# Optimization experiments

Hardware: AMD Instinct MI355X
Metric: run time of the kernel (lower is better)

## Reference

```python
import jax, jax.numpy as jnp
import numpy as np

BN_EPS = 1e-5


def _conv1x1(x, w, b):
    # x: (B,C,H,W), w: (O,C) -> (B,O,H,W)
    return jnp.einsum('bchw,oc->bohw', x, w) + b[None, :, None, None]


def _maxpool2x2(x):
    b, c, h, w = x.shape
    return x.reshape(b, c, h // 2, 2, w // 2, 2).max(axis=(3, 5))


def _minmax(a, axis):
    mn = a.min(axis=axis, keepdims=True)
    mx = a.max(axis=axis, keepdims=True)
    return (a - mn) / (mx - mn)


def _gaussian_bias(row, dh, dw):
    # Vectorized version of the original per-row numpy double loop.
    sigma = max(1, int(min(dh, dw) / 10))
    j = jnp.arange(row)
    cx = ((j // 4) // dw).astype(jnp.float32)   # floor(j/4/down_col)
    cy = ((j // 4) % dw).astype(jnp.float32)    # floor(j/4) % down_col
    mx = jnp.arange(dh, dtype=jnp.float32)[None, :, None]
    my = jnp.arange(dw, dtype=jnp.float32)[None, None, :]
    d2 = (mx - cx[:, None, None]) ** 2 + (my - cy[:, None, None]) ** 2
    return (-d2 / (2.0 * sigma * sigma)).reshape(row, dh * dw)  # (row, col)


def reference(x, g_w, g_b, theta_w, theta_b, phi_w, phi_b, w_w, w_b,
              bn_gamma, bn_beta, bn_mean, bn_var):
    b, c, H, W = x.shape
    ic = g_w.shape[0]
    dh, dw = H // 2, W // 2
    row, col = H * W, dh * dw

    g_x = _maxpool2x2(_conv1x1(x, g_w, g_b)).reshape(b, ic, col).transpose(0, 2, 1)  # (b,col,ic)
    theta = _conv1x1(x, theta_w, theta_b).reshape(b, ic, row).transpose(0, 2, 1)     # (b,row,ic)
    phi = _maxpool2x2(_conv1x1(x, phi_w, phi_b)).reshape(b, ic, col)                 # (b,ic,col)

    f = jnp.einsum('bri,bic->brc', theta, phi)  # (b,row,col)
    temp = _gaussian_bias(row, dh, dw)[None]    # (1,row,col), same for all batch

    f = (_minmax(f, -1) - 1.0) + (_minmax(temp, -1) - 1.0)
    f_div_C = jax.nn.softmax(f, axis=-1)

    g_x = _minmax(g_x, 1)  # min/max over positions
    y = jnp.einsum('brc,bci->bri', f_div_C, g_x)        # (b,row,ic)
    y = y.transpose(0, 2, 1).reshape(b, ic, H, W)

    W_y = _conv1x1(y, w_w, w_b)
    W_y = bn_gamma[None, :, None, None] * (W_y - bn_mean[None, :, None, None]) \
        * jax.lax.rsqrt(bn_var + BN_EPS)[None, :, None, None] + bn_beta[None, :, None, None]
    return W_y + x


def setup_inputs() -> dict:
    key = jax.random.key(0)
    ks = jax.random.split(key, 13)
    B, C, IC, H, W = 8, 64, 32, 64, 64
    s = 0.1
    return {
        'x': jax.random.normal(ks[0], (B, C, H, W), jnp.float32),
        'g_w': jax.random.normal(ks[1], (IC, C), jnp.float32) * s,
        'g_b': jax.random.normal(ks[2], (IC,), jnp.float32) * s,
        'theta_w': jax.random.normal(ks[3], (IC, C), jnp.float32) * s,
        'theta_b': jax.random.normal(ks[4], (IC,), jnp.float32) * s,
        'phi_w': jax.random.normal(ks[5], (IC, C), jnp.float32) * s,
        'phi_b': jax.random.normal(ks[6], (IC,), jnp.float32) * s,
        'w_w': jax.random.normal(ks[7], (C, IC), jnp.float32) * s,
        'w_b': jax.random.normal(ks[8], (C,), jnp.float32) * s,
        'bn_gamma': jax.random.uniform(ks[9], (C,), jnp.float32, 0.5, 1.5),
        'bn_beta': jax.random.normal(ks[10], (C,), jnp.float32) * s,
        'bn_mean': jax.random.normal(ks[11], (C,), jnp.float32) * s,
        'bn_var': jax.random.uniform(ks[12], (C,), jnp.float32, 0.5, 1.5),
    }
```

## Files before the change

kernel.cpp:

```cpp
#include <hip/hip_runtime.h>
#include <math.h>

#define RFL(x) __builtin_amdgcn_readfirstlane(x)

static constexpr int Bn = 8, Cn = 64, ICn = 32, Hn = 64, Wn = 64;
static constexpr int ROW = Hn * Wn;
static constexpr int COLn = 1024;

static constexpr size_t OFF_THETA = 0;
static constexpr size_t OFF_PHI   = (size_t)Bn * ROW * ICn;
static constexpr size_t OFF_G     = OFF_PHI + (size_t)Bn * ICn * COLn;
static constexpr size_t OFF_Y     = OFF_G + (size_t)Bn * COLn * ICn;
static constexpr size_t OFF_GMN   = OFF_Y + (size_t)Bn * ROW * ICn;
static constexpr size_t OFF_GINV  = OFF_GMN + (size_t)Bn * ICn;

__device__ __forceinline__ void gload_lds16(const float* src, float* ldsbase) {
    __builtin_amdgcn_global_load_lds(
        (const __attribute__((address_space(1))) unsigned int*)(const void*)src,
        (__attribute__((address_space(3))) unsigned int*)(void*)ldsbase, 16, 0, 0);
}

__global__ __launch_bounds__(256) void k_conv3(
    const float* __restrict__ x,
    const float* __restrict__ wth, const float* __restrict__ bth,
    const float* __restrict__ wph, const float* __restrict__ bph,
    const float* __restrict__ wg,  const float* __restrict__ bg,
    float* __restrict__ theta, float* __restrict__ phi, float* __restrict__ g)
{
    const int tid  = threadIdx.x;
    const int lane = tid & 63;
    const int ty   = RFL(tid >> 6);
    const int b    = blockIdx.z;
    const int pc   = blockIdx.x * 64 + lane;
    const int phh  = pc >> 5, pww = pc & 31;
    const int o0   = (blockIdx.y * 4 + ty) * 4;

    const float* xb = x + (size_t)b * Cn * ROW;
    const int pos0 = (2 * phh) * Wn + 2 * pww;

    float accT[4][4], accP[4][4], accG[4][4];
    #pragma unroll
    for (int j = 0; j < 4; ++j)
        #pragma unroll
        for (int q = 0; q < 4; ++q) { accT[j][q] = 0.f; accP[j][q] = 0.f; accG[j][q] = 0.f; }

    float2 pf0[8], pf1[8];
    #pragma unroll
    for (int i = 0; i < 8; ++i) {
        const float* xc = xb + (size_t)i * ROW + pos0;
        pf0[i] = *(const float2*)xc;
        pf1[i] = *(const float2*)(xc + Wn);
    }
    #pragma unroll 1
    for (int cb = 0; cb < Cn; cb += 8) {
        float2 c0[8], c1[8];
        #pragma unroll
        for (int i = 0; i < 8; ++i) { c0[i] = pf0[i]; c1[i] = pf1[i]; }
        if (cb + 8 < Cn) {
            #pragma unroll
            for (int i = 0; i < 8; ++i) {
                const float* xc = xb + (size_t)(cb + 8 + i) * ROW + pos0;
                pf0[i] = *(const float2*)xc;
                pf1[i] = *(const float2*)(xc + Wn);
            }
        }
        #pragma unroll
        for (int i = 0; i < 8; ++i) {
            const int c = cb + i;
            const float xv0 = c0[i].x, xv1 = c0[i].y, xv2 = c1[i].x, xv3 = c1[i].y;
            #pragma unroll
            for (int j = 0; j < 4; ++j) {
                const int o = o0 + j;
                const float wt  = wth[o * Cn + c];
                const float wp  = wph[o * Cn + c];
                const float wgv = wg [o * Cn + c];
                accT[j][0] = fmaf(wt, xv0, accT[j][0]); accT[j][1] = fmaf(wt, xv1, accT[j][1]);
                accT[j][2] = fmaf(wt, xv2, accT[j][2]); accT[j][3] = fmaf(wt, xv3, accT[j][3]);
                accP[j][0] = fmaf(wp, xv0, accP[j][0]); accP[j][1] = fmaf(wp, xv1, accP[j][1]);
                accP[j][2] = fmaf(wp, xv2, accP[j][2]); accP[j][3] = fmaf(wp, xv3, accP[j][3]);
                accG[j][0] = fmaf(wgv, xv0, accG[j][0]); accG[j][1] = fmaf(wgv, xv1, accG[j][1]);
                accG[j][2] = fmaf(wgv, xv2, accG[j][2]); accG[j][3] = fmaf(wgv, xv3, accG[j][3]);
            }
        }
    }

    const int prow[4] = {pos0, pos0 + 1, pos0 + Wn, pos0 + Wn + 1};
    const float4 bt4 = *(const float4*)(bth + o0);
    #pragma unroll
    for (int q = 0; q < 4; ++q) {
        float4 tv;
        tv.x = accT[0][q] + bt4.x; tv.y = accT[1][q] + bt4.y;
        tv.z = accT[2][q] + bt4.z; tv.w = accT[3][q] + bt4.w;
        *(float4*)&theta[((size_t)b * ROW + prow[q]) * ICn + o0] = tv;
    }
    float4 gv;
    #pragma unroll
    for (int j = 0; j < 4; ++j) {
        const int o = o0 + j;
        float mp = fmaxf(fmaxf(accP[j][0], accP[j][1]), fmaxf(accP[j][2], accP[j][3]));
        phi[((size_t)b * ICn + o) * COLn + pc] = mp + bph[o];
        float mg = fmaxf(fmaxf(accG[j][0], accG[j][1]), fmaxf(accG[j][2], accG[j][3]));
        (&gv.x)[j] = mg + bg[o];
    }
    *(float4*)&g[((size_t)b * COLn + pc) * ICn + o0] = gv;
}

__global__ __launch_bounds__(64) void k_gminmax(
    const float* __restrict__ g, float* __restrict__ gmn, float* __restrict__ ginv)
{
    const int ic = blockIdx.x, b = blockIdx.y, lane = threadIdx.x;
    float mn = 3.4e38f, mx = -3.4e38f;
    for (int i = 0; i < COLn; i += 64) {
        float v = g[((size_t)b * COLn + i + lane) * ICn + ic];
        mn = fminf(mn, v); mx = fmaxf(mx, v);
    }
    #pragma unroll
    for (int m = 1; m < 64; m <<= 1) {
        mn = fminf(mn, __shfl_xor(mn, m));
        mx = fmaxf(mx, __shfl_xor(mx, m));
    }
    if (lane == 0) {
        gmn[b * ICn + ic] = mn;
        ginv[b * ICn + ic] = 1.0f / (mx - mn);
    }
}

#define RPW 4
#define CCH 256
#define PCOL(c) ((c) ^ ((((c) >> 5) & 7) << 2))

__global__ __launch_bounds__(256, 5) void k_attn(
    const float* __restrict__ theta, const float* __restrict__ phi,
    const float* __restrict__ g, const float* __restrict__ gmn,
    const float* __restrict__ ginv, float* __restrict__ y)
{
    __shared__ float smem[32 * CCH];

    const int tid  = threadIdx.x;
    const int lane = tid & 63;
    const int wid  = RFL(tid >> 6);
    const int b    = blockIdx.y;
    const int icq  = lane & 7;
    const int csplit = lane >> 3;
    const int colbase = lane * 4;

    const float* phiB = phi + (size_t)b * ICn * COLn;
    const float* gB   = g + (size_t)b * COLn * ICn;
    const float4 gmn4 = *(const float4*)(gmn + b * ICn + icq * 4);
    const float4 giv4 = *(const float4*)(ginv + b * ICn + icq * 4);

    const int row0 = blockIdx.x * 16 + wid * RPW;
    const float* thB = theta + ((size_t)b * ROW + row0) * ICn;
    float* const pSw = smem + wid * (RPW * CCH);

    float4 f4[RPW][4];
    #pragma unroll
    for (int r = 0; r < RPW; ++r) {
        f4[r][0] = make_float4(0.f, 0.f, 0.f, 0.f);
        f4[r][1] = make_float4(0.f, 0.f, 0.f, 0.f);
        f4[r][2] = make_float4(0.f, 0.f, 0.f, 0.f);
        f4[r][3] = make_float4(0.f, 0.f, 0.f, 0.f);
    }

    #define PHASEA_CH(CH) { \
        __syncthreads(); \
        _Pragma("unroll") \
        for (int i = 0; i < 8; ++i) { \
            const int k = wid * 8 + i; \
            gload_lds16(phiB + (size_t)k * COLn + (CH) * CCH + lane * 4, &smem[k * CCH]); \
        } \
        __syncthreads(); \
        _Pragma("unroll 8") \
        for (int k = 0; k < 32; ++k) { \
            float4 pv = *(const float4*)&smem[k * CCH + colbase]; \
            _Pragma("unroll") \
            for (int r = 0; r < RPW; ++r) { \
                const float t = thB[r * ICn + k]; \
                f4[r][CH].x = fmaf(t, pv.x, f4[r][CH].x); \
                f4[r][CH].y = fmaf(t, pv.y, f4[r][CH].y); \
                f4[r][CH].z = fmaf(t, pv.z, f4[r][CH].z); \
                f4[r][CH].w = fmaf(t, pv.w, f4[r][CH].w); \
            } \
        } }
    PHASEA_CH(0) PHASEA_CH(1) PHASEA_CH(2) PHASEA_CH(3)
    #undef PHASEA_CH

    float rinv[RPW];
    #pragma unroll
    for (int r = 0; r < RPW; ++r) {
        const int row = row0 + r;
        float mn = 3.4e38f, mx = -3.4e38f;
        #pragma unroll
        for (int ch = 0; ch < 4; ++ch) {
            float4 v = f4[r][ch];
            mn = fminf(mn, fminf(fminf(v.x, v.y), fminf(v.z, v.w)));
            mx = fmaxf(mx, fmaxf(fmaxf(v.x, v.y), fmaxf(v.z, v.w)));
        }
        #pragma unroll
        for (int m = 1; m < 64; m <<= 1) {
            mn = fminf(mn, __shfl_xor(mn, m));
            mx = fmaxf(mx, __shfl_xor(mx, m));
        }
        const float finv = 1.0f / (mx - mn);
        const float cx = (float)(row >> 7);
        const float cy = (float)((row >> 2) & 31);
        const float mdx = fmaxf(cx * cx, (31.0f - cx) * (31.0f - cx));
        const float mdy = fmaxf(cy * cy, (31.0f - cy) * (31.0f - cy));
        const float dinv = 1.0f / (mdx + mdy);
        const float c0 = -1.0f - mn * finv;

        float dx2[4], dy2[4];
        #pragma unroll
        for (int u = 0; u < 4; ++u) {
            const float dx = (float)(u * 8 + csplit) - cx;
            dx2[u] = dx * dx;
            const float dy = (float)(icq * 4 + u) - cy;
            dy2[u] = dy * dy;
        }
        float s0 = 0.f, s1 = 0.f;
        #pragma unroll
        for (int ch = 0; ch < 4; ++ch) {
            float4 v = f4[r][ch];
            v.x = __expf(fmaf(v.x, finv, fmaf(dx2[ch] + dy2[0], -dinv, c0)));
            v.y = __expf(fmaf(v.y, finv, fmaf(dx2[ch] + dy2[1], -dinv, c0)));
            v.z = __expf(fmaf(v.z, finv, fmaf(dx2[ch] + dy2[2], -dinv, c0)));
            v.w = __expf(fmaf(v.w, finv, fmaf(dx2[ch] + dy2[3], -dinv, c0)));
            f4[r][ch] = v;
            s0 += v.x + v.y; s1 += v.z + v.w;
        }
        float s = s0 + s1;
        #pragma unroll
        for (int m = 1; m < 64; m <<= 1) s += __shfl_xor(s, m);
        rinv[r] = 1.0f / s;
    }

    __syncthreads();

    float4 y4[RPW];
    #pragma unroll
    for (int r = 0; r < RPW; ++r) y4[r] = make_float4(0.f, 0.f, 0.f, 0.f);

    #define PHASEC_CH(CH) { \
        _Pragma("unroll") \
        for (int r = 0; r < RPW; ++r) \
            *(float4*)&pSw[r * CCH + PCOL(colbase)] = f4[r][CH]; \
        asm volatile("s_waitcnt lgkmcnt(0)" ::: "memory"); \
        const float* gch = gB + (size_t)(CH) * CCH * ICn + icq * 4; \
        _Pragma("unroll 2") \
        for (int cc4 = 0; cc4 < 32; cc4 += 4) { \
            const int cl = csplit * 32 + cc4; \
            float4 pb[RPW]; \
            _Pragma("unroll") \
            for (int r = 0; r < RPW; ++r) \
                pb[r] = *(const float4*)&pSw[r * CCH + PCOL(cl)]; \
            const float* gp = gch + (size_t)cl * ICn; \
            float4 g4; \
            _Pragma("unroll") \
            for (int u = 0; u < 4; ++u) { \
                g4 = *(const float4*)(gp + u * ICn); \
                _Pragma("unroll") \
                for (int r = 0; r < RPW; ++r) { \
                    const float pv = (&pb[r].x)[u]; \
                    y4[r].x = fmaf(pv, g4.x, y4[r].x); \
                    y4[r].y = fmaf(pv, g4.y, y4[r].y); \
                    y4[r].z = fmaf(pv, g4.z, y4[r].z); \
                    y4[r].w = fmaf(pv, g4.w, y4[r].w); \
                } \
            } \
        } \
        asm volatile("" ::: "memory"); }
    PHASEC_CH(0) PHASEC_CH(1) PHASEC_CH(2) PHASEC_CH(3)
    #undef PHASEC_CH

    #pragma unroll
    for (int r = 0; r < RPW; ++r) {
        float4 v = y4[r];
        #pragma unroll
        for (int m = 8; m < 64; m <<= 1) {
            v.x += __shfl_xor(v.x, m);
            v.y += __shfl_xor(v.y, m);
            v.z += __shfl_xor(v.z, m);
            v.w += __shfl_xor(v.w, m);
        }
        if (csplit == 0) {
            const float rs = rinv[r];
            float4 o;
            o.x = v.x * rs * giv4.x - gmn4.x * giv4.x;
            o.y = v.y * rs * giv4.y - gmn4.y * giv4.y;
            o.z = v.z * rs * giv4.z - gmn4.z * giv4.z;
            o.w = v.w * rs * giv4.w - gmn4.w * giv4.w;
            *(float4*)&y[((size_t)b * ROW + row0 + r) * ICn + icq * 4] = o;
        }
    }
}

__global__ __launch_bounds__(256) void k_out(
    const float* __restrict__ y, const float* __restrict__ x,
    const float* __restrict__ ww, const float* __restrict__ wb,
    const float* __restrict__ gam, const float* __restrict__ bet,
    const float* __restrict__ mean, const float* __restrict__ var,
    float* __restrict__ out)
{
    const int tid = threadIdx.x, lane = tid & 63;
    const int ty = RFL(tid >> 6);
    const int b = blockIdx.y;
    const int p = blockIdx.x * 64 + lane;

    const float* yr = y + ((size_t)b * ROW + p) * ICn;
    float4 yv[8];
    #pragma unroll
    for (int i = 0; i < 8; ++i) yv[i] = *(const float4*)(yr + i * 4);

    const int o0 = ty * 16;
    #pragma unroll 4
    for (int oo = 0; oo < 16; ++oo) {
        const int o = o0 + oo;
        const float* wr = ww + o * ICn;
        float acc = 0.f;
        #pragma unroll
        for (int i = 0; i < 8; ++i) {
            acc = fmaf(wr[i * 4 + 0], yv[i].x, acc);
            acc = fmaf(wr[i * 4 + 1], yv[i].y, acc);
            acc = fmaf(wr[i * 4 + 2], yv[i].z, acc);
            acc = fmaf(wr[i * 4 + 3], yv[i].w, acc);
        }
        const float s = gam[o] * rsqrtf(var[o] + 1e-5f);
        const float res = s * (acc + wb[o] - mean[o]) + bet[o]
                        + x[((size_t)(b * Cn + o)) * ROW + p];
        out[((size_t)(b * Cn + o)) * ROW + p] = res;
    }
}

extern "C" void kernel_launch(void* const* d_in, const int* in_sizes, int n_in,
                              void* d_out, int out_size, void* d_ws, size_t ws_size,
                              hipStream_t stream) {
    (void)in_sizes; (void)n_in; (void)out_size; (void)ws_size;
    const float* x    = (const float*)d_in[0];
    const float* g_w  = (const float*)d_in[1];
    const float* g_b  = (const float*)d_in[2];
    const float* th_w = (const float*)d_in[3];
    const float* th_b = (const float*)d_in[4];
    const float* ph_w = (const float*)d_in[5];
    const float* ph_b = (const float*)d_in[6];
    const float* w_w  = (const float*)d_in[7];
    const float* w_b  = (const float*)d_in[8];
    const float* bng  = (const float*)d_in[9];
    const float* bnb  = (const float*)d_in[10];
    const float* bnm  = (const float*)d_in[11];
    const float* bnv  = (const float*)d_in[12];
    float* out = (float*)d_out;
    float* ws  = (float*)d_ws;

    float* theta = ws + OFF_THETA;
    float* phi   = ws + OFF_PHI;
    float* g     = ws + OFF_G;
    float* y     = ws + OFF_Y;
    float* gmn   = ws + OFF_GMN;
    float* ginv  = ws + OFF_GINV;

    hipLaunchKernelGGL(k_conv3, dim3(16, 2, 8), dim3(256), 0, stream,
                       x, th_w, th_b, ph_w, ph_b, g_w, g_b, theta, phi, g);
    hipLaunchKernelGGL(k_gminmax, dim3(32, 8), dim3(64), 0, stream, g, gmn, ginv);
    hipLaunchKernelGGL(k_attn, dim3(256, 8), dim3(256), 0, stream,
                       theta, phi, g, gmn, ginv, y);
    hipLaunchKernelGGL(k_out, dim3(64, 8), dim3(256), 0, stream,
                       y, x, w_w, w_b, bng, bnb, bnm, bnv, out);
}
```

Measured before the change: 209.4 us.

## Rebalance work splits across conv, minmax, attention and output kernels

Each conv3 thread now covers 2 output channels instead of 4, with twice as many blocks, and the output kernel is split over more blocks with 8 channels per wave. The g min/max reduction moves to one 256-thread block per 4 channels, using float4 loads and an LDS cross-wave reduce. The attention kernel doubles rows per wave to 8 so each phi tile staged in LDS is reused more. It also gives the probability buffer its own LDS region, which drops one barrier. In exchange the attention kernel uses more registers and LDS, lowering occupancy to 2 blocks per CU, and some kernels get less work per thread.

```diff
diff --git a/kernel.cpp b/kernel.cpp
--- a/kernel.cpp
+++ b/kernel.cpp
@@ -33,14 +33,14 @@
     const int b    = blockIdx.z;
     const int pc   = blockIdx.x * 64 + lane;
     const int phh  = pc >> 5, pww = pc & 31;
-    const int o0   = (blockIdx.y * 4 + ty) * 4;
+    const int o0   = blockIdx.y * 8 + ty * 2;
 
     const float* xb = x + (size_t)b * Cn * ROW;
     const int pos0 = (2 * phh) * Wn + 2 * pww;
 
-    float accT[4][4], accP[4][4], accG[4][4];
-    #pragma unroll
-    for (int j = 0; j < 4; ++j)
+    float accT[2][4], accP[2][4], accG[2][4];
+    #pragma unroll
+    for (int j = 0; j < 2; ++j)
         #pragma unroll
         for (int q = 0; q < 4; ++q) { accT[j][q] = 0.f; accP[j][q] = 0.f; accG[j][q] = 0.f; }
 
@@ -69,7 +69,7 @@
             const int c = cb + i;
             const float xv0 = c0[i].x, xv1 = c0[i].y, xv2 = c1[i].x, xv3 = c1[i].y;
             #pragma unroll
-            for (int j = 0; j < 4; ++j) {
+            for (int j = 0; j < 2; ++j) {
                 const int o = o0 + j;
                 const float wt  = wth[o * Cn + c];
                 const float wp  = wph[o * Cn + c];
@@ -85,56 +85,75 @@
     }
 
     const int prow[4] = {pos0, pos0 + 1, pos0 + Wn, pos0 + Wn + 1};
-    const float4 bt4 = *(const float4*)(bth + o0);
+    const float bt0 = bth[o0], bt1 = bth[o0 + 1];
     #pragma unroll
     for (int q = 0; q < 4; ++q) {
-        float4 tv;
-        tv.x = accT[0][q] + bt4.x; tv.y = accT[1][q] + bt4.y;
-        tv.z = accT[2][q] + bt4.z; tv.w = accT[3][q] + bt4.w;
-        *(float4*)&theta[((size_t)b * ROW + prow[q]) * ICn + o0] = tv;
-    }
-    float4 gv;
-    #pragma unroll
-    for (int j = 0; j < 4; ++j) {
+        float2 tv;
+        tv.x = accT[0][q] + bt0; tv.y = accT[1][q] + bt1;
+        *(float2*)&theta[((size_t)b * ROW + prow[q]) * ICn + o0] = tv;
+    }
+    float2 gv;
+    #pragma unroll
+    for (int j = 0; j < 2; ++j) {
         const int o = o0 + j;
         float mp = fmaxf(fmaxf(accP[j][0], accP[j][1]), fmaxf(accP[j][2], accP[j][3]));
         phi[((size_t)b * ICn + o) * COLn + pc] = mp + bph[o];
         float mg = fmaxf(fmaxf(accG[j][0], accG[j][1]), fmaxf(accG[j][2], accG[j][3]));
         (&gv.x)[j] = mg + bg[o];
     }
-    *(float4*)&g[((size_t)b * COLn + pc) * ICn + o0] = gv;
-}
-
-__global__ __launch_bounds__(64) void k_gminmax(
+    *(float2*)&g[((size_t)b * COLn + pc) * ICn + o0] = gv;
+}
+
+__global__ __launch_bounds__(256) void k_gminmax(
     const float* __restrict__ g, float* __restrict__ gmn, float* __restrict__ ginv)
 {
-    const int ic = blockIdx.x, b = blockIdx.y, lane = threadIdx.x;
-    float mn = 3.4e38f, mx = -3.4e38f;
-    for (int i = 0; i < COLn; i += 64) {
-        float v = g[((size_t)b * COLn + i + lane) * ICn + ic];
-        mn = fminf(mn, v); mx = fmaxf(mx, v);
+    __shared__ float red[2][4][4];
+    const int tid = threadIdx.x;
+    const int icq = blockIdx.x & 7, b = blockIdx.x >> 3;
+    float4 mn4 = make_float4(3.4e38f, 3.4e38f, 3.4e38f, 3.4e38f);
+    float4 mx4 = make_float4(-3.4e38f, -3.4e38f, -3.4e38f, -3.4e38f);
+    #pragma unroll
+    for (int i = 0; i < 4; ++i) {
+        float4 v = *(const float4*)&g[((size_t)b * COLn + i * 256 + tid) * ICn + icq * 4];
+        mn4.x = fminf(mn4.x, v.x); mn4.y = fminf(mn4.y, v.y);
+        mn4.z = fminf(mn4.z, v.z); mn4.w = fminf(mn4.w, v.w);
+        mx4.x = fmaxf(mx4.x, v.x); mx4.y = fmaxf(mx4.y, v.y);
+        mx4.z = fmaxf(mx4.z, v.z); mx4.w = fmaxf(mx4.w, v.w);
     }
     #pragma unroll
     for (int m = 1; m < 64; m <<= 1) {
-        mn = fminf(mn, __shfl_xor(mn, m));
-        mx = fmaxf(mx, __shfl_xor(mx, m));
-    }
-    if (lane == 0) {
-        gmn[b * ICn + ic] = mn;
-        ginv[b * ICn + ic] = 1.0f / (mx - mn);
-    }
-}
-
-#define RPW 4
+        mn4.x = fminf(mn4.x, __shfl_xor(mn4.x, m)); mx4.x = fmaxf(mx4.x, __shfl_xor(mx4.x, m));
+        mn4.y = fminf(mn4.y, __shfl_xor(mn4.y, m)); mx4.y = fmaxf(mx4.y, __shfl_xor(mx4.y, m));
+        mn4.z = fminf(mn4.z, __shfl_xor(mn4.z, m)); mx4.z = fmaxf(mx4.z, __shfl_xor(mx4.z, m));
+        mn4.w = fminf(mn4.w, __shfl_xor(mn4.w, m)); mx4.w = fmaxf(mx4.w, __shfl_xor(mx4.w, m));
+    }
+    const int wv = tid >> 6;
+    if ((tid & 63) == 0) {
+        red[0][wv][0] = mn4.x; red[0][wv][1] = mn4.y; red[0][wv][2] = mn4.z; red[0][wv][3] = mn4.w;
+        red[1][wv][0] = mx4.x; red[1][wv][1] = mx4.y; red[1][wv][2] = mx4.z; red[1][wv][3] = mx4.w;
+    }
+    __syncthreads();
+    if (tid < 4) {
+        float mn = fminf(fminf(red[0][0][tid], red[0][1][tid]),
+                         fminf(red[0][2][tid], red[0][3][tid]));
+        float mx = fmaxf(fmaxf(red[1][0][tid], red[1][1][tid]),
+                         fmaxf(red[1][2][tid], red[1][3][tid]));
+        gmn[b * ICn + icq * 4 + tid] = mn;
+        ginv[b * ICn + icq * 4 + tid] = 1.0f / (mx - mn);
+    }
+}
+
+#define RPW 8
 #define CCH 256
 #define PCOL(c) ((c) ^ ((((c) >> 5) & 7) << 2))
 
-__global__ __launch_bounds__(256, 5) void k_attn(
+__global__ __launch_bounds__(256, 2) void k_attn(
     const float* __restrict__ theta, const float* __restrict__ phi,
     const float* __restrict__ g, const float* __restrict__ gmn,
     const float* __restrict__ ginv, float* __restrict__ y)
 {
-    __shared__ float smem[32 * CCH];
+    __shared__ float phiS[32 * CCH];
+    __shared__ float pS[4][RPW][CCH];
 
     const int tid  = threadIdx.x;
     const int lane = tid & 63;
@@ -149,9 +168,9 @@
     const float4 gmn4 = *(const float4*)(gmn + b * ICn + icq * 4);
     const float4 giv4 = *(const float4*)(ginv + b * ICn + icq * 4);
 
-    const int row0 = blockIdx.x * 16 + wid * RPW;
+    const int row0 = blockIdx.x * 32 + wid * RPW;
     const float* thB = theta + ((size_t)b * ROW + row0) * ICn;
-    float* const pSw = smem + wid * (RPW * CCH);
+    float* const pSw = &pS[wid][0][0];
 
     float4 f4[RPW][4];
     #pragma unroll
@@ -167,12 +186,12 @@
         _Pragma("unroll") \
         for (int i = 0; i < 8; ++i) { \
             const int k = wid * 8 + i; \
-            gload_lds16(phiB + (size_t)k * COLn + (CH) * CCH + lane * 4, &smem[k * CCH]); \
+            gload_lds16(phiB + (size_t)k * COLn + (CH) * CCH + lane * 4, &phiS[k * CCH]); \
         } \
         __syncthreads(); \
         _Pragma("unroll 8") \
         for (int k = 0; k < 32; ++k) { \
-            float4 pv = *(const float4*)&smem[k * CCH + colbase]; \
+            float4 pv = *(const float4*)&phiS[k * CCH + colbase]; \
             _Pragma("unroll") \
             for (int r = 0; r < RPW; ++r) { \
                 const float t = thB[r * ICn + k]; \
@@ -233,8 +252,6 @@
         for (int m = 1; m < 64; m <<= 1) s += __shfl_xor(s, m);
         rinv[r] = 1.0f / s;
     }
-
-    __syncthreads();
 
     float4 y4[RPW];
     #pragma unroll
@@ -303,17 +320,17 @@
 {
     const int tid = threadIdx.x, lane = tid & 63;
     const int ty = RFL(tid >> 6);
-    const int b = blockIdx.y;
+    const int b = blockIdx.z;
     const int p = blockIdx.x * 64 + lane;
+    const int o0 = (blockIdx.y * 4 + ty) * 8;
 
     const float* yr = y + ((size_t)b * ROW + p) * ICn;
     float4 yv[8];
     #pragma unroll
     for (int i = 0; i < 8; ++i) yv[i] = *(const float4*)(yr + i * 4);
 
-    const int o0 = ty * 16;
-    #pragma unroll 4
-    for (int oo = 0; oo < 16; ++oo) {
+    #pragma unroll
+    for (int oo = 0; oo < 8; ++oo) {
         const int o = o0 + oo;
         const float* wr = ww + o * ICn;
         float acc = 0.f;
@@ -358,11 +375,11 @@
     float* gmn   = ws + OFF_GMN;
     float* ginv  = ws + OFF_GINV;
 
-    hipLaunchKernelGGL(k_conv3, dim3(16, 2, 8), dim3(256), 0, stream,
+    hipLaunchKernelGGL(k_conv3, dim3(16, 4, 8), dim3(256), 0, stream,
                        x, th_w, th_b, ph_w, ph_b, g_w, g_b, theta, phi, g);
-    hipLaunchKernelGGL(k_gminmax, dim3(32, 8), dim3(64), 0, stream, g, gmn, ginv);
-    hipLaunchKernelGGL(k_attn, dim3(256, 8), dim3(256), 0, stream,
+    hipLaunchKernelGGL(k_gminmax, dim3(64), dim3(256), 0, stream, g, gmn, ginv);
+    hipLaunchKernelGGL(k_attn, dim3(128, 8), dim3(256), 0, stream,
                        theta, phi, g, gmn, ginv, y);
-    hipLaunchKernelGGL(k_out, dim3(64, 8), dim3(256), 0, stream,
+    hipLaunchKernelGGL(k_out, dim3(64, 2, 8), dim3(256), 0, stream,
                        y, x, w_w, w_b, bng, bnb, bnm, bnv, out);
 }
```

After: 176.6 us. 1.19x faster.
